# Kernel optimization log

Hardware: AMD Instinct MI355X
Metric: run time of the kernel (lower is better)

The kernel has to match this reference:

```python
import jax, jax.numpy as jnp
import numpy as np

N_KNOTS = 10
NEXPERTS = 1
NC = 8
STEP = 1.0 / (N_KNOTS - 1.0)
BN_EPS = 1e-5


def _spline_matrix(n, step):
    # natural cubic spline second-derivative solve matrix (precalc in torch code)
    mat = 4.0 * np.eye(n - 2)
    np.fill_diagonal(mat[1:, :-1], 1.0)
    np.fill_diagonal(mat[:-1, 1:], 1.0)
    A = 6.0 * np.linalg.inv(mat) / step ** 2
    z = np.zeros((1, n - 2))
    A = np.vstack([z, A, z])                      # [n, n-2]
    B = np.zeros((n - 2, n))
    np.fill_diagonal(B, 1.0)
    np.fill_diagonal(B[:, 1:], -2.0)
    np.fill_diagonal(B[:, 2:], 1.0)
    return jnp.asarray(A @ B, dtype=jnp.float32)  # [n, n]


def _conv(x, w, b, stride=2):
    y = jax.lax.conv_general_dilated(x, w, (stride, stride), 'VALID',
                                     dimension_numbers=('NCHW', 'OIHW', 'NCHW'))
    return y + b[None, :, None, None]


def _bn(x, g, be):
    # training-mode batchnorm (module default)
    m = x.mean(axis=(0, 2, 3), keepdims=True)
    v = x.var(axis=(0, 2, 3), keepdims=True)
    return g[None, :, None, None] * (x - m) * jax.lax.rsqrt(v + BN_EPS) + be[None, :, None, None]


def _interpolate(ys, mat):
    # ys: [..., n] -> cubic coeffs a,b,c,d each [..., n-1]
    h = STEP
    M = jnp.einsum('ij,...j->...i', mat, ys)
    a = (M[..., 1:] - M[..., :-1]) / (6.0 * h)
    b = M[..., :-1] / 2.0
    c = (ys[..., 1:] - ys[..., :-1]) / h - (M[..., 1:] + 2.0 * M[..., :-1]) * (h / 6.0)
    d = ys[..., :-1]
    return a, b, c, d


def _apply(coeffs, x):
    # coeffs: 4-tuple each [..., n-1]; x: [..., P] with matching leading dims
    a, b, c, d = coeffs
    xi = jnp.clip(jnp.floor(x / STEP), 0.0, N_KNOTS - 2.0)
    xf = x - xi * STEP
    idx = xi.astype(jnp.int32)
    ag = jnp.take_along_axis(a, idx, axis=-1)
    bg = jnp.take_along_axis(b, idx, axis=-1)
    cg = jnp.take_along_axis(c, idx, axis=-1)
    dg = jnp.take_along_axis(d, idx, axis=-1)
    return ((ag * xf + bg) * xf + cg) * xf + dg


def forward(x, w1, b1, w2, b2, g2, be2, w3, b3, g3, be3, w4, b4, g4, be4,
            w5, b5, g5, be5, fc1_w, fc1_b, fc2_w, fc2_b):
    B, C, H, W = x.shape
    small = x if (H, W) == (256, 256) else jax.image.resize(x, (B, C, 256, 256), 'bilinear')
    h = jax.nn.relu(_conv(small, w1, b1))
    h = _bn(jax.nn.relu(_conv(h, w2, b2)), g2, be2)
    h = _bn(jax.nn.relu(_conv(h, w3, b3)), g3, be3)
    h = _bn(jax.nn.relu(_conv(h, w4, b4)), g4, be4)
    h = _bn(jax.nn.relu(_conv(h, w5, b5)), g5, be5)   # [B, 16nc, 7, 7]
    h = h.mean(axis=(2, 3))                            # avgpool 7 -> [B, 16nc]
    h = jax.nn.relu(h @ fc1_w.T + fc1_b)
    ys = (h @ fc2_w.T + fc2_b).reshape(B, NEXPERTS, 3, N_KNOTS)
    identity = jnp.arange(N_KNOTS, dtype=jnp.float32) / (N_KNOTS - 1.0)
    ysn = ys + identity                                # residual spline
    mat = _spline_matrix(N_KNOTS, STEP)
    coeffs = _interpolate(ysn, mat)                    # each [B,E,3,n-1]
    # per-pixel spline eval at original resolution
    px = jnp.broadcast_to(x.reshape(B, 1, 3, H * W), (B, NEXPERTS, 3, H * W))
    out = _apply(coeffs, px).reshape(B, NEXPERTS, 3, H, W)
    out = jnp.transpose(out, (1, 0, 2, 3, 4))          # [E,B,3,H,W]
    # spline curves sampled at xs = arange(0,1,1/255) (255 points; detached in torch)
    xs = jnp.arange(0.0, 1.0, 1.0 / 255.0, dtype=jnp.float32)
    xs_b = jnp.broadcast_to(xs, (B, NEXPERTS, 3, xs.shape[0]))
    splines = jnp.transpose(_apply(coeffs, xs_b), (1, 0, 2, 3))  # [E,B,3,255]
    return out, splines


def setup_inputs() -> dict:
    key = jax.random.key(0)
    ks = jax.random.split(key, 16)
    n, nc, E = N_KNOTS, NC, NEXPERTS
    d = {}
    d['x'] = jax.random.uniform(ks[0], (8, 3, 1024, 1024), dtype=jnp.float32)
    d['w1'] = jax.random.normal(ks[1], (nc, 3, 3, 3), jnp.float32) * 0.1
    d['b1'] = jnp.zeros((nc,), jnp.float32)
    chans = [nc, 2 * nc, 4 * nc, 8 * nc, 16 * nc]
    for i, (ci, co) in enumerate(zip(chans[:-1], chans[1:]), start=2):
        d[f'w{i}'] = jax.random.normal(ks[i], (co, ci, 3, 3), jnp.float32) * 0.1
        d[f'b{i}'] = jnp.zeros((co,), jnp.float32)
        d[f'g{i}'] = jnp.ones((co,), jnp.float32)
        d[f'be{i}'] = jnp.zeros((co,), jnp.float32)
    d['fc1_w'] = jax.random.normal(ks[10], (16 * nc, 16 * nc), jnp.float32) * 0.05
    d['fc1_b'] = jnp.zeros((16 * nc,), jnp.float32)
    d['fc2_w'] = jax.random.normal(ks[11], (3 * n * E, 16 * nc), jnp.float32) * 0.05
    d['fc2_b'] = jnp.zeros((3 * n * E,), jnp.float32)
    return d


def reference(x, w1, b1, w2, b2, g2, be2, w3, b3, g3, be3, w4, b4, g4, be4,
              w5, b5, g5, be5, fc1_w, fc1_b, fc2_w, fc2_b):
    return forward(x, w1, b1, w2, b2, g2, be2, w3, b3, g3, be3, w4, b4, g4, be4,
                   w5, b5, g5, be5, fc1_w, fc1_b, fc2_w, fc2_b)
```

## Files before the change

### kernel.cpp

```cpp
#include <hip/hip_runtime.h>

#define SPLINE_OFF 25165824
#define STEP_F (1.0f/9.0f)

typedef float f32x4 __attribute__((ext_vector_type(4)));

__global__ __launch_bounds__(256) void resize_k(const float* __restrict__ x,
                                                float* __restrict__ sm) {
    __shared__ float vsum[1024];
    const int blk = blockIdx.x;
    const int plane = blk >> 8;
    const int orow = blk & 255;
    const int t = threadIdx.x;

    const float W[8] = {0.125f,0.375f,0.625f,0.875f,0.875f,0.625f,0.375f,0.125f};
    const float* p = x + (size_t)plane * 1048576 + t * 4;
    const int r0 = 4 * orow - 2;
    float ax = 0.f, ay = 0.f, az = 0.f, aw = 0.f;
    if (r0 >= 0 && r0 + 7 <= 1023) {
        #pragma unroll
        for (int k = 0; k < 8; k++) {
            const float4 v = *(const float4*)(p + (r0 + k) * 1024);
            const float w = W[k] * 0.25f;
            ax = fmaf(v.x, w, ax); ay = fmaf(v.y, w, ay);
            az = fmaf(v.z, w, az); aw = fmaf(v.w, w, aw);
        }
    } else {
        float wsum = 0.f;
        #pragma unroll
        for (int k = 0; k < 8; k++) {
            const int r = r0 + k;
            if (r >= 0 && r < 1024) {
                const float4 v = *(const float4*)(p + r * 1024);
                ax = fmaf(v.x, W[k], ax); ay = fmaf(v.y, W[k], ay);
                az = fmaf(v.z, W[k], az); aw = fmaf(v.w, W[k], aw);
                wsum += W[k];
            }
        }
        const float inv = 1.f / wsum;
        ax *= inv; ay *= inv; az *= inv; aw *= inv;
    }
    vsum[4 * t + 0] = ax; vsum[4 * t + 1] = ay;
    vsum[4 * t + 2] = az; vsum[4 * t + 3] = aw;
    __syncthreads();

    const int c0 = 4 * t - 2;
    float acc = 0.f;
    if (c0 >= 0 && c0 + 7 <= 1023) {
        #pragma unroll
        for (int k = 0; k < 8; k++)
            acc = fmaf(vsum[c0 + k], W[k] * 0.25f, acc);
    } else {
        float wsum = 0.f;
        #pragma unroll
        for (int k = 0; k < 8; k++) {
            const int c = c0 + k;
            if (c >= 0 && c < 1024) { acc = fmaf(vsum[c], W[k], acc); wsum += W[k]; }
        }
        acc /= wsum;
    }
    sm[(size_t)blk * 256 + t] = acc;
}

template<int CIN, int COUT, int INW, int OUTW, int NCO, int CISPLIT, int PIX,
         int NTPREV, int NTOUT, bool INBN, bool STATS, bool WRITE>
__global__ __launch_bounds__(PIX * CISPLIT) void conv_k(
    const float* __restrict__ in, const float* __restrict__ w,
    const float* __restrict__ bias,
    const float* __restrict__ gam, const float* __restrict__ be,
    const float* __restrict__ pS, const float* __restrict__ pQ, float invN,
    float* __restrict__ out,
    float* __restrict__ pSo, float* __restrict__ pQo)
{
    constexpr int BLOCK = PIX * CISPLIT;
    constexpr int CPS = CIN / CISPLIT;
    constexpr int COG = COUT / NCO;

    __shared__ float wsm[NCO][CIN * 9];
    __shared__ float scs[CIN], shs[CIN];
    __shared__ float wrow[NCO][CIN];
    __shared__ float cadd[NCO];
    __shared__ float part[CISPLIT][PIX][NCO];
    __shared__ float red[NCO][2][PIX / 64];
    __shared__ float sredS[BLOCK], sredQ[BLOCK];

    const int tid = threadIdx.x;
    const int p   = tid & (PIX - 1);
    const int cs  = tid / PIX;
    const int bc  = blockIdx.y;
    const int b   = bc / COG;
    const int co0 = (bc % COG) * NCO;

    if constexpr (INBN) {
        constexpr int GRP = BLOCK / CIN;
        constexpr int TERMS = 8 * NTPREV;
        const int ci = tid % CIN;
        const int gi = tid / CIN;
        float s = 0.f, q = 0.f;
        for (int j = gi; j < TERMS; j += GRP) {
            const int bb = j / NTPREV, tl = j - bb * NTPREV;
            const int a = (bb * CIN + ci) * NTPREV + tl;
            s += pS[a]; q += pQ[a];
        }
        sredS[gi * CIN + ci] = s;
        sredQ[gi * CIN + ci] = q;
        __syncthreads();
        if (tid < CIN) {
            float ts = 0.f, tq = 0.f;
            #pragma unroll
            for (int g2 = 0; g2 < GRP; g2++) {
                ts += sredS[g2 * CIN + tid];
                tq += sredQ[g2 * CIN + tid];
            }
            const float m = ts * invN;
            const float v = tq * invN - m * m;
            const float sc = gam[tid] * rsqrtf(v + 1e-5f);
            scs[tid] = sc;
            shs[tid] = be[tid] - m * sc;
        }
        __syncthreads();
    }

    for (int i = tid; i < NCO * CIN * 9; i += BLOCK) {
        int n = i / (CIN * 9), r = i - n * (CIN * 9), ci = r / 9;
        float wv = w[(co0 + n) * CIN * 9 + r];
        wsm[n][r] = INBN ? wv * scs[ci] : wv;
    }
    if constexpr (INBN) {
        for (int i = tid; i < NCO * CIN; i += BLOCK) {
            int n = i / CIN, ci = i - n * CIN;
            const float* wp = w + ((co0 + n) * CIN + ci) * 9;
            float s = 0.f;
            #pragma unroll
            for (int k = 0; k < 9; k++) s += wp[k];
            wrow[n][ci] = s;
        }
    }
    __syncthreads();
    if (tid < NCO) {
        float c = bias[co0 + tid];
        if constexpr (INBN) {
            for (int ci = 0; ci < CIN; ci++) c = fmaf(wrow[tid][ci], shs[ci], c);
        }
        cadd[tid] = c;
    }
    __syncthreads();

    const int npix = OUTW * OUTW;
    const int pg = blockIdx.x * PIX + p;
    float acc[NCO];
    #pragma unroll
    for (int n = 0; n < NCO; n++) acc[n] = 0.f;

    if (pg < npix) {
        const int oh = pg / OUTW, ow = pg - oh * OUTW;
        const float* ib = in + ((size_t)(b * CIN) + cs * CPS) * INW * INW
                             + (size_t)(2 * oh) * INW + 2 * ow;
        #pragma unroll 4
        for (int ci = 0; ci < CPS; ci++) {
            const float* ip = ib + (size_t)ci * INW * INW;
            const int cw = (cs * CPS + ci) * 9;
            #pragma unroll
            for (int kh = 0; kh < 3; kh++) {
                const float* r = ip + kh * INW;
                #pragma unroll
                for (int kw = 0; kw < 3; kw++) {
                    const float xv = r[kw];
                    #pragma unroll
                    for (int n = 0; n < NCO; n++)
                        acc[n] = fmaf(xv, wsm[n][cw + kh * 3 + kw], acc[n]);
                }
            }
        }
    }

    float val[NCO];
    #pragma unroll
    for (int n = 0; n < NCO; n++) val[n] = 0.f;

    if constexpr (CISPLIT > 1) {
        #pragma unroll
        for (int n = 0; n < NCO; n++) part[cs][p][n] = acc[n];
        __syncthreads();
    }

    if (cs == 0) {
        #pragma unroll
        for (int n = 0; n < NCO; n++) {
            float s = acc[n];
            if constexpr (CISPLIT > 1) {
                #pragma unroll
                for (int q = 1; q < CISPLIT; q++) s += part[q][p][n];
            }
            if (pg < npix) {
                val[n] = fmaxf(s + cadd[n], 0.f);
                if constexpr (WRITE)
                    out[(size_t)(b * COUT + co0 + n) * npix + pg] = val[n];
            }
        }
    }

    if constexpr (STATS) {
        if (cs == 0) {
            #pragma unroll
            for (int n = 0; n < NCO; n++) {
                float s = val[n], sq = val[n] * val[n];
                #pragma unroll
                for (int off = 32; off > 0; off >>= 1) {
                    s  += __shfl_down(s, off);
                    sq += __shfl_down(sq, off);
                }
                if ((tid & 63) == 0) { red[n][0][tid >> 6] = s; red[n][1][tid >> 6] = sq; }
            }
        }
        __syncthreads();
        if (tid == 0) {
            #pragma unroll
            for (int n = 0; n < NCO; n++) {
                float ts = 0.f, tq = 0.f;
                #pragma unroll
                for (int i = 0; i < PIX / 64; i++) { ts += red[n][0][i]; tq += red[n][1][i]; }
                const int idx = (b * COUT + co0 + n) * NTOUT + blockIdx.x;
                pSo[idx] = ts;
                pQo[idx] = tq;
            }
        }
    }
}

__global__ __launch_bounds__(256) void fc_spline_k(
    const float* __restrict__ pS5, const float* __restrict__ pQ5,
    const float* __restrict__ g5, const float* __restrict__ be5,
    const float* __restrict__ fc1w, const float* __restrict__ fc1b,
    const float* __restrict__ fc2w, const float* __restrict__ fc2b,
    float* __restrict__ coeff_out, float* __restrict__ splines_out)
{
    __shared__ float sc5[128], sh5[128];
    __shared__ float h[1024];
    __shared__ float h1v[1024];
    __shared__ float ysn[240];
    __shared__ float coef[24][36];

    const int t = threadIdx.x;

    if (t < 128) {
        float s = 0.f, q = 0.f;
        #pragma unroll
        for (int b = 0; b < 8; b++) { s += pS5[b * 128 + t]; q += pQ5[b * 128 + t]; }
        float m = s * (1.f / 392.f);
        float v = q * (1.f / 392.f) - m * m;
        float sc = g5[t] * rsqrtf(v + 1e-5f);
        sc5[t] = sc;
        sh5[t] = be5[t] - m * sc;
    }
    __syncthreads();

    for (int i = t; i < 1024; i += 256) {
        int c = i & 127;
        h[i] = fmaf(sc5[c], pS5[i] * (1.f / 49.f), sh5[c]);
    }
    __syncthreads();

    for (int i = t; i < 1024; i += 256) {
        int b = i >> 7, j = i & 127;
        float acc = fc1b[j];
        for (int c = 0; c < 128; c++)
            acc = fmaf(h[(b << 7) + c], fc1w[(j << 7) + c], acc);
        h1v[i] = fmaxf(acc, 0.f);
    }
    __syncthreads();

    if (t < 240) {
        int b = t / 30, k = t % 30;
        float acc = fc2b[k];
        for (int j = 0; j < 128; j++)
            acc = fmaf(h1v[(b << 7) + j], fc2w[(k << 7) + j], acc);
        ysn[t] = acc + (float)(k % 10) * STEP_F;
    }
    __syncthreads();

    if (t < 24) {
        float y[10];
        #pragma unroll
        for (int i = 0; i < 10; i++) y[i] = ysn[t * 10 + i];
        float rhs[9], cp[9], dp[9];
        #pragma unroll
        for (int i = 1; i <= 8; i++)
            rhs[i] = 486.f * (y[i - 1] - 2.f * y[i] + y[i + 1]);
        cp[1] = 0.25f; dp[1] = rhs[1] * 0.25f;
        #pragma unroll
        for (int i = 2; i <= 8; i++) {
            float m = 1.f / (4.f - cp[i - 1]);
            cp[i] = m;
            dp[i] = (rhs[i] - dp[i - 1]) * m;
        }
        float M[10];
        M[0] = 0.f; M[9] = 0.f;
        M[8] = dp[8];
        #pragma unroll
        for (int i = 7; i >= 1; i--) M[i] = dp[i] - cp[i] * M[i + 1];
        #pragma unroll
        for (int i = 0; i < 9; i++) {
            float a = (M[i + 1] - M[i]) * 1.5f;
            float bb = M[i] * 0.5f;
            float cc = (y[i + 1] - y[i]) * 9.f - (M[i + 1] + 2.f * M[i]) * (STEP_F / 6.f);
            float dd = y[i];
            coef[t][i] = a; coef[t][9 + i] = bb; coef[t][18 + i] = cc; coef[t][27 + i] = dd;
            coeff_out[t * 36 + i] = a;
            coeff_out[t * 36 + 9 + i] = bb;
            coeff_out[t * 36 + 18 + i] = cc;
            coeff_out[t * 36 + 27 + i] = dd;
        }
    }
    __syncthreads();

    for (int i = t; i < 24 * 255; i += 256) {
        int bc = i / 255, k = i - bc * 255;
        float xv = (float)k * (1.0f / 255.0f);
        float xi = floorf(xv * 9.0f);
        xi = fminf(fmaxf(xi, 0.f), 8.f);
        int ix = (int)xi;
        float xf = xv - xi * STEP_F;
        const float* cf = coef[bc];
        splines_out[i] = fmaf(fmaf(fmaf(cf[ix], xf, cf[9 + ix]), xf, cf[18 + ix]), xf, cf[27 + ix]);
    }
}

__global__ __launch_bounds__(256) void apply_k(const float* __restrict__ x,
                                               const float* __restrict__ coeff,
                                               float* __restrict__ out)
{
    __shared__ float cf[36];
    const int blk = blockIdx.x;
    const int plane = blk >> 10;
    const int t = threadIdx.x;
    if (t < 36) cf[t] = coeff[plane * 36 + t];
    __syncthreads();

    size_t base = (size_t)blk * 1024 + (size_t)t * 4;
    float4 v = *(const float4*)(x + base);
    f32x4 o;
    #pragma unroll
    for (int k = 0; k < 4; k++) {
        float xv = (k == 0) ? v.x : (k == 1) ? v.y : (k == 2) ? v.z : v.w;
        float xi = floorf(xv * 9.0f);
        xi = fminf(fmaxf(xi, 0.f), 8.f);
        int ix = (int)xi;
        float xf = xv - xi * STEP_F;
        o[k] = fmaf(fmaf(fmaf(cf[ix], xf, cf[9 + ix]), xf, cf[18 + ix]), xf, cf[27 + ix]);
    }
    __builtin_nontemporal_store(o, (f32x4*)(out + base));
}

extern "C" void kernel_launch(void* const* d_in, const int* in_sizes, int n_in,
                              void* d_out, int out_size, void* d_ws, size_t ws_size,
                              hipStream_t stream) {
    (void)in_sizes; (void)n_in; (void)out_size; (void)ws_size;

    const float* x    = (const float*)d_in[0];
    const float* w1   = (const float*)d_in[1];
    const float* b1   = (const float*)d_in[2];
    const float* w2   = (const float*)d_in[3];
    const float* b2   = (const float*)d_in[4];
    const float* g2   = (const float*)d_in[5];
    const float* be2  = (const float*)d_in[6];
    const float* w3   = (const float*)d_in[7];
    const float* b3   = (const float*)d_in[8];
    const float* g3   = (const float*)d_in[9];
    const float* be3  = (const float*)d_in[10];
    const float* w4   = (const float*)d_in[11];
    const float* b4   = (const float*)d_in[12];
    const float* g4   = (const float*)d_in[13];
    const float* be4  = (const float*)d_in[14];
    const float* w5   = (const float*)d_in[15];
    const float* b5   = (const float*)d_in[16];
    const float* g5   = (const float*)d_in[17];
    const float* be5  = (const float*)d_in[18];
    const float* fc1w = (const float*)d_in[19];
    const float* fc1b = (const float*)d_in[20];
    const float* fc2w = (const float*)d_in[21];
    const float* fc2b = (const float*)d_in[22];

    float* out = (float*)d_out;
    float* wsf = (float*)d_ws;

    float* pS2 = wsf + 0;
    float* pQ2 = wsf + 2048;
    float* pS3 = wsf + 4096;
    float* pQ3 = wsf + 5120;
    float* pS4 = wsf + 6144;
    float* pQ4 = wsf + 6656;
    float* pS5 = wsf + 7168;
    float* pQ5 = wsf + 8192;
    float* coeff = wsf + 9216;

    float* sm  = out;
    float* h1  = out + 1572864;
    float* h2  = out + 2605120;
    float* h3  = out + 3113152;
    float* h4  = out + 3359168;

    resize_k<<<6144, 256, 0, stream>>>(x, sm);

    conv_k<3, 8, 256, 127, 2, 1, 256, 1, 1, false, false, true>
        <<<dim3(64, 32), 256, 0, stream>>>(sm, w1, b1, nullptr, nullptr,
                                           nullptr, nullptr, 0.f,
                                           h1, nullptr, nullptr);
    conv_k<8, 16, 127, 63, 2, 1, 256, 1, 16, false, true, true>
        <<<dim3(16, 64), 256, 0, stream>>>(h1, w2, b2, nullptr, nullptr,
                                           nullptr, nullptr, 0.f,
                                           h2, pS2, pQ2);
    conv_k<16, 32, 63, 31, 2, 1, 256, 16, 4, true, true, true>
        <<<dim3(4, 128), 256, 0, stream>>>(h2, w3, b3, g2, be2,
                                           pS2, pQ2, 1.0f / 31752.0f,
                                           h3, pS3, pQ3);
    conv_k<32, 64, 31, 15, 2, 2, 256, 4, 1, true, true, true>
        <<<dim3(1, 256), 512, 0, stream>>>(h3, w4, b4, g3, be3,
                                           pS3, pQ3, 1.0f / 7688.0f,
                                           h4, pS4, pQ4);
    conv_k<64, 128, 15, 7, 2, 4, 64, 1, 1, true, true, false>
        <<<dim3(1, 512), 256, 0, stream>>>(h4, w5, b5, g4, be4,
                                           pS4, pQ4, 1.0f / 1800.0f,
                                           nullptr, pS5, pQ5);

    fc_spline_k<<<1, 256, 0, stream>>>(pS5, pQ5, g5, be5,
                                       fc1w, fc1b, fc2w, fc2b,
                                       coeff, out + SPLINE_OFF);

    apply_k<<<24576, 256, 0, stream>>>(x, coeff, out);
}
```

Measured before the change: 132.1 us.

## Fuse conv1 and conv2 into tiled kernel, batch resize rows, raise CI split

A new tiled kernel fuses conv1 and conv2. It stages the resized input tile and the conv1 output in shared memory, so the h1 intermediate never goes to global memory, and it emits per-tile BN statistics. The resize kernel now computes two output rows per block and shares the overlapping input rows, which cuts redundant global loads. The later convs use larger input-channel splits and therefore bigger blocks, trading more shared-memory reduction for more parallelism per block.

```diff
diff --git a/kernel.cpp b/kernel.cpp
--- a/kernel.cpp
+++ b/kernel.cpp
@@ -7,62 +7,174 @@
 
 __global__ __launch_bounds__(256) void resize_k(const float* __restrict__ x,
                                                 float* __restrict__ sm) {
-    __shared__ float vsum[1024];
+    __shared__ float vs[2][1024];
     const int blk = blockIdx.x;
-    const int plane = blk >> 8;
-    const int orow = blk & 255;
+    const int plane = blk >> 7;
+    const int orA = (blk & 127) * 2;
     const int t = threadIdx.x;
 
     const float W[8] = {0.125f,0.375f,0.625f,0.875f,0.875f,0.625f,0.375f,0.125f};
     const float* p = x + (size_t)plane * 1048576 + t * 4;
-    const int r0 = 4 * orow - 2;
-    float ax = 0.f, ay = 0.f, az = 0.f, aw = 0.f;
-    if (r0 >= 0 && r0 + 7 <= 1023) {
-        #pragma unroll
-        for (int k = 0; k < 8; k++) {
-            const float4 v = *(const float4*)(p + (r0 + k) * 1024);
-            const float w = W[k] * 0.25f;
-            ax = fmaf(v.x, w, ax); ay = fmaf(v.y, w, ay);
-            az = fmaf(v.z, w, az); aw = fmaf(v.w, w, aw);
+    const int rA = 4 * orA - 2;
+
+    float a0x=0.f,a0y=0.f,a0z=0.f,a0w=0.f;
+    float a1x=0.f,a1y=0.f,a1z=0.f,a1w=0.f;
+
+    if (rA >= 0 && rA + 11 <= 1023) {
+        #pragma unroll
+        for (int k = 0; k < 12; k++) {
+            const float4 v = *(const float4*)(p + (size_t)(rA + k) * 1024);
+            if (k < 8) {
+                const float w = W[k] * 0.25f;
+                a0x = fmaf(v.x, w, a0x); a0y = fmaf(v.y, w, a0y);
+                a0z = fmaf(v.z, w, a0z); a0w = fmaf(v.w, w, a0w);
+            }
+            if (k >= 4) {
+                const float w = W[k - 4] * 0.25f;
+                a1x = fmaf(v.x, w, a1x); a1y = fmaf(v.y, w, a1y);
+                a1z = fmaf(v.z, w, a1z); a1w = fmaf(v.w, w, a1w);
+            }
         }
     } else {
-        float wsum = 0.f;
-        #pragma unroll
-        for (int k = 0; k < 8; k++) {
-            const int r = r0 + k;
-            if (r >= 0 && r < 1024) {
-                const float4 v = *(const float4*)(p + r * 1024);
-                ax = fmaf(v.x, W[k], ax); ay = fmaf(v.y, W[k], ay);
-                az = fmaf(v.z, W[k], az); aw = fmaf(v.w, W[k], aw);
-                wsum += W[k];
-            }
-        }
-        const float inv = 1.f / wsum;
-        ax *= inv; ay *= inv; az *= inv; aw *= inv;
-    }
-    vsum[4 * t + 0] = ax; vsum[4 * t + 1] = ay;
-    vsum[4 * t + 2] = az; vsum[4 * t + 3] = aw;
+        #pragma unroll
+        for (int o = 0; o < 2; o++) {
+            const int r0 = 4 * (orA + o) - 2;
+            float bx=0.f,by=0.f,bz=0.f,bw=0.f,wsum=0.f;
+            #pragma unroll
+            for (int k = 0; k < 8; k++) {
+                const int r = r0 + k;
+                if (r >= 0 && r < 1024) {
+                    const float4 v = *(const float4*)(p + (size_t)r * 1024);
+                    bx = fmaf(v.x, W[k], bx); by = fmaf(v.y, W[k], by);
+                    bz = fmaf(v.z, W[k], bz); bw = fmaf(v.w, W[k], bw);
+                    wsum += W[k];
+                }
+            }
+            const float inv = 1.f / wsum;
+            if (o == 0) { a0x=bx*inv; a0y=by*inv; a0z=bz*inv; a0w=bw*inv; }
+            else        { a1x=bx*inv; a1y=by*inv; a1z=bz*inv; a1w=bw*inv; }
+        }
+    }
+    vs[0][4*t+0]=a0x; vs[0][4*t+1]=a0y; vs[0][4*t+2]=a0z; vs[0][4*t+3]=a0w;
+    vs[1][4*t+0]=a1x; vs[1][4*t+1]=a1y; vs[1][4*t+2]=a1z; vs[1][4*t+3]=a1w;
     __syncthreads();
 
     const int c0 = 4 * t - 2;
-    float acc = 0.f;
-    if (c0 >= 0 && c0 + 7 <= 1023) {
-        #pragma unroll
-        for (int k = 0; k < 8; k++)
-            acc = fmaf(vsum[c0 + k], W[k] * 0.25f, acc);
-    } else {
-        float wsum = 0.f;
-        #pragma unroll
-        for (int k = 0; k < 8; k++) {
-            const int c = c0 + k;
-            if (c >= 0 && c < 1024) { acc = fmaf(vsum[c], W[k], acc); wsum += W[k]; }
-        }
-        acc /= wsum;
-    }
-    sm[(size_t)blk * 256 + t] = acc;
+    #pragma unroll
+    for (int o = 0; o < 2; o++) {
+        float acc = 0.f;
+        if (c0 >= 0 && c0 + 7 <= 1023) {
+            #pragma unroll
+            for (int k = 0; k < 8; k++)
+                acc = fmaf(vs[o][c0 + k], W[k] * 0.25f, acc);
+        } else {
+            float wsum = 0.f;
+            #pragma unroll
+            for (int k = 0; k < 8; k++) {
+                const int c = c0 + k;
+                if (c >= 0 && c < 1024) { acc = fmaf(vs[o][c], W[k], acc); wsum += W[k]; }
+            }
+            acc /= wsum;
+        }
+        sm[((size_t)plane * 256 + orA + o) * 256 + t] = acc;
+    }
 }
 
-template<int CIN, int COUT, int INW, int OUTW, int NCO, int CISPLIT, int PIX,
+__global__ __launch_bounds__(256) void c1c2_k(
+    const float* __restrict__ sm,
+    const float* __restrict__ w1, const float* __restrict__ b1,
+    const float* __restrict__ w2, const float* __restrict__ b2,
+    float* __restrict__ h2, float* __restrict__ pS2, float* __restrict__ pQ2)
+{
+    __shared__ float smT[3 * 1225];
+    __shared__ float c1T[8 * 289];
+    __shared__ float w1s[216];
+    __shared__ float w2s[1152];
+    __shared__ float bs[24];
+
+    const int tile = blockIdx.x;
+    const int b    = blockIdx.y;
+    const int tx = tile & 7, ty = tile >> 3;
+    const int R0 = ty * 8, C0 = tx * 8;
+    const int t = threadIdx.x;
+
+    if (t < 216) w1s[t] = w1[t];
+    for (int i = t; i < 1152; i += 256) w2s[i] = w2[i];
+    if (t < 8) bs[t] = b1[t];
+    else if (t < 24) bs[t] = b2[t - 8];
+
+    const int r0 = 4 * R0, c0 = 4 * C0;
+    for (int i = t; i < 3675; i += 256) {
+        const int ch = i / 1225, rem = i - ch * 1225;
+        const int r = rem / 35, c = rem - r * 35;
+        const int gr = r0 + r, gc = c0 + c;
+        float v = 0.f;
+        if (gr < 256 && gc < 256)
+            v = sm[((size_t)(b * 3 + ch) << 16) + (gr << 8) + gc];
+        smT[i] = v;
+    }
+    __syncthreads();
+
+    for (int i = t; i < 2312; i += 256) {
+        const int co = i / 289, pp = i - co * 289;
+        const int r = pp / 17, c = pp - r * 17;
+        float acc = bs[co];
+        #pragma unroll
+        for (int ch = 0; ch < 3; ch++) {
+            const float* sp = &smT[ch * 1225 + (2 * r) * 35 + 2 * c];
+            const float* wp = &w1s[co * 27 + ch * 9];
+            #pragma unroll
+            for (int kh = 0; kh < 3; kh++) {
+                acc = fmaf(sp[kh * 35 + 0], wp[kh * 3 + 0], acc);
+                acc = fmaf(sp[kh * 35 + 1], wp[kh * 3 + 1], acc);
+                acc = fmaf(sp[kh * 35 + 2], wp[kh * 3 + 2], acc);
+            }
+        }
+        c1T[i] = fmaxf(acc, 0.f);
+    }
+    __syncthreads();
+
+    const int px = t & 63, cog = t >> 6;
+    const int pr = px >> 3, pc = px & 7;
+    const bool valid = (R0 + pr < 63) && (C0 + pc < 63);
+    float vals[4];
+    #pragma unroll
+    for (int k = 0; k < 4; k++) {
+        const int co = cog * 4 + k;
+        float acc = bs[8 + co];
+        #pragma unroll
+        for (int ci = 0; ci < 8; ci++) {
+            const float* cp = &c1T[ci * 289 + (2 * pr) * 17 + 2 * pc];
+            const float* wp = &w2s[co * 72 + ci * 9];
+            #pragma unroll
+            for (int kh = 0; kh < 3; kh++) {
+                acc = fmaf(cp[kh * 17 + 0], wp[kh * 3 + 0], acc);
+                acc = fmaf(cp[kh * 17 + 1], wp[kh * 3 + 1], acc);
+                acc = fmaf(cp[kh * 17 + 2], wp[kh * 3 + 2], acc);
+            }
+        }
+        const float v = valid ? fmaxf(acc, 0.f) : 0.f;
+        vals[k] = v;
+        if (valid)
+            h2[(size_t)(b * 16 + co) * 3969 + (R0 + pr) * 63 + (C0 + pc)] = v;
+    }
+    #pragma unroll
+    for (int k = 0; k < 4; k++) {
+        float s = vals[k], q = vals[k] * vals[k];
+        #pragma unroll
+        for (int off = 32; off > 0; off >>= 1) {
+            s += __shfl_down(s, off);
+            q += __shfl_down(q, off);
+        }
+        if (px == 0) {
+            const int co = cog * 4 + k;
+            pS2[(b * 16 + co) * 64 + tile] = s;
+            pQ2[(b * 16 + co) * 64 + tile] = q;
+        }
+    }
+}
+
+template<int CIN, int COUT, int INW, int OUTW, int CISPLIT, int PIX,
          int NTPREV, int NTOUT, bool INBN, bool STATS, bool WRITE>
 __global__ __launch_bounds__(PIX * CISPLIT) void conv_k(
     const float* __restrict__ in, const float* __restrict__ w,
@@ -74,14 +186,14 @@
 {
     constexpr int BLOCK = PIX * CISPLIT;
     constexpr int CPS = CIN / CISPLIT;
-    constexpr int COG = COUT / NCO;
-
-    __shared__ float wsm[NCO][CIN * 9];
+    constexpr int COG = COUT / 2;
+
+    __shared__ float wsm[2][CIN * 9];
     __shared__ float scs[CIN], shs[CIN];
-    __shared__ float wrow[NCO][CIN];
-    __shared__ float cadd[NCO];
-    __shared__ float part[CISPLIT][PIX][NCO];
-    __shared__ float red[NCO][2][PIX / 64];
+    __shared__ float wrow[2][CIN];
+    __shared__ float cadd[2];
+    __shared__ float part[CISPLIT][PIX][2];
+    __shared__ float red[2][2][PIX / 64];
     __shared__ float sredS[BLOCK], sredQ[BLOCK];
 
     const int tid = threadIdx.x;
@@ -89,7 +201,7 @@
     const int cs  = tid / PIX;
     const int bc  = blockIdx.y;
     const int b   = bc / COG;
-    const int co0 = (bc % COG) * NCO;
+    const int co0 = (bc % COG) * 2;
 
     if constexpr (INBN) {
         constexpr int GRP = BLOCK / CIN;
@@ -121,14 +233,14 @@
         __syncthreads();
     }
 
-    for (int i = tid; i < NCO * CIN * 9; i += BLOCK) {
-        int n = i / (CIN * 9), r = i - n * (CIN * 9), ci = r / 9;
-        float wv = w[(co0 + n) * CIN * 9 + r];
+    for (int i = tid; i < 2 * CIN * 9; i += BLOCK) {
+        const int n = i / (CIN * 9), r = i - n * (CIN * 9), ci = r / 9;
+        const float wv = w[(co0 + n) * CIN * 9 + r];
         wsm[n][r] = INBN ? wv * scs[ci] : wv;
     }
     if constexpr (INBN) {
-        for (int i = tid; i < NCO * CIN; i += BLOCK) {
-            int n = i / CIN, ci = i - n * CIN;
+        for (int i = tid; i < 2 * CIN; i += BLOCK) {
+            const int n = i / CIN, ci = i - n * CIN;
             const float* wp = w + ((co0 + n) * CIN + ci) * 9;
             float s = 0.f;
             #pragma unroll
@@ -137,7 +249,7 @@
         }
     }
     __syncthreads();
-    if (tid < NCO) {
+    if (tid < 2) {
         float c = bias[co0 + tid];
         if constexpr (INBN) {
             for (int ci = 0; ci < CIN; ci++) c = fmaf(wrow[tid][ci], shs[ci], c);
@@ -148,17 +260,14 @@
 
     const int npix = OUTW * OUTW;
     const int pg = blockIdx.x * PIX + p;
-    float acc[NCO];
-    #pragma unroll
-    for (int n = 0; n < NCO; n++) acc[n] = 0.f;
-
+    float a0 = 0.f, a1 = 0.f;
     if (pg < npix) {
         const int oh = pg / OUTW, ow = pg - oh * OUTW;
-        const float* ib = in + ((size_t)(b * CIN) + cs * CPS) * INW * INW
+        const float* ib = in + ((size_t)(b * CIN) + cs * CPS) * (INW * INW)
                              + (size_t)(2 * oh) * INW + 2 * ow;
         #pragma unroll 4
         for (int ci = 0; ci < CPS; ci++) {
-            const float* ip = ib + (size_t)ci * INW * INW;
+            const float* ip = ib + (size_t)ci * (INW * INW);
             const int cw = (cs * CPS + ci) * 9;
             #pragma unroll
             for (int kh = 0; kh < 3; kh++) {
@@ -166,64 +275,59 @@
                 #pragma unroll
                 for (int kw = 0; kw < 3; kw++) {
                     const float xv = r[kw];
-                    #pragma unroll
-                    for (int n = 0; n < NCO; n++)
-                        acc[n] = fmaf(xv, wsm[n][cw + kh * 3 + kw], acc[n]);
+                    a0 = fmaf(xv, wsm[0][cw + kh * 3 + kw], a0);
+                    a1 = fmaf(xv, wsm[1][cw + kh * 3 + kw], a1);
                 }
             }
         }
     }
 
-    float val[NCO];
-    #pragma unroll
-    for (int n = 0; n < NCO; n++) val[n] = 0.f;
-
+    float v0 = 0.f, v1 = 0.f;
     if constexpr (CISPLIT > 1) {
-        #pragma unroll
-        for (int n = 0; n < NCO; n++) part[cs][p][n] = acc[n];
+        part[cs][p][0] = a0; part[cs][p][1] = a1;
         __syncthreads();
     }
-
     if (cs == 0) {
-        #pragma unroll
-        for (int n = 0; n < NCO; n++) {
-            float s = acc[n];
-            if constexpr (CISPLIT > 1) {
-                #pragma unroll
-                for (int q = 1; q < CISPLIT; q++) s += part[q][p][n];
-            }
-            if (pg < npix) {
-                val[n] = fmaxf(s + cadd[n], 0.f);
-                if constexpr (WRITE)
-                    out[(size_t)(b * COUT + co0 + n) * npix + pg] = val[n];
+        float s0 = a0, s1 = a1;
+        if constexpr (CISPLIT > 1) {
+            #pragma unroll
+            for (int q = 1; q < CISPLIT; q++) { s0 += part[q][p][0]; s1 += part[q][p][1]; }
+        }
+        if (pg < npix) {
+            v0 = fmaxf(s0 + cadd[0], 0.f);
+            v1 = fmaxf(s1 + cadd[1], 0.f);
+            if constexpr (WRITE) {
+                out[(size_t)(b * COUT + co0) * npix + pg] = v0;
+                out[(size_t)(b * COUT + co0 + 1) * npix + pg] = v1;
             }
         }
     }
 
     if constexpr (STATS) {
         if (cs == 0) {
-            #pragma unroll
-            for (int n = 0; n < NCO; n++) {
-                float s = val[n], sq = val[n] * val[n];
-                #pragma unroll
-                for (int off = 32; off > 0; off >>= 1) {
-                    s  += __shfl_down(s, off);
-                    sq += __shfl_down(sq, off);
-                }
-                if ((tid & 63) == 0) { red[n][0][tid >> 6] = s; red[n][1][tid >> 6] = sq; }
+            float sA = v0, qA = v0 * v0, sB = v1, qB = v1 * v1;
+            #pragma unroll
+            for (int off = 32; off > 0; off >>= 1) {
+                sA += __shfl_down(sA, off); qA += __shfl_down(qA, off);
+                sB += __shfl_down(sB, off); qB += __shfl_down(qB, off);
+            }
+            if ((tid & 63) == 0) {
+                red[0][0][tid >> 6] = sA; red[0][1][tid >> 6] = qA;
+                red[1][0][tid >> 6] = sB; red[1][1][tid >> 6] = qB;
             }
         }
         __syncthreads();
         if (tid == 0) {
-            #pragma unroll
-            for (int n = 0; n < NCO; n++) {
-                float ts = 0.f, tq = 0.f;
-                #pragma unroll
-                for (int i = 0; i < PIX / 64; i++) { ts += red[n][0][i]; tq += red[n][1][i]; }
-                const int idx = (b * COUT + co0 + n) * NTOUT + blockIdx.x;
-                pSo[idx] = ts;
-                pQo[idx] = tq;
-            }
+            float tsA = 0.f, tqA = 0.f, tsB = 0.f, tqB = 0.f;
+            #pragma unroll
+            for (int i = 0; i < PIX / 64; i++) {
+                tsA += red[0][0][i]; tqA += red[0][1][i];
+                tsB += red[1][0][i]; tqB += red[1][1][i];
+            }
+            pSo[(b * COUT + co0) * NTOUT + blockIdx.x] = tsA;
+            pQo[(b * COUT + co0) * NTOUT + blockIdx.x] = tqA;
+            pSo[(b * COUT + co0 + 1) * NTOUT + blockIdx.x] = tsB;
+            pQo[(b * COUT + co0 + 1) * NTOUT + blockIdx.x] = tqB;
         }
     }
 }
@@ -385,41 +489,34 @@
     float* wsf = (float*)d_ws;
 
     float* pS2 = wsf + 0;
-    float* pQ2 = wsf + 2048;
-    float* pS3 = wsf + 4096;
-    float* pQ3 = wsf + 5120;
-    float* pS4 = wsf + 6144;
-    float* pQ4 = wsf + 6656;
-    float* pS5 = wsf + 7168;
-    float* pQ5 = wsf + 8192;
-    float* coeff = wsf + 9216;
+    float* pQ2 = wsf + 8192;
+    float* pS3 = wsf + 16384;
+    float* pQ3 = wsf + 17408;
+    float* pS4 = wsf + 18432;
+    float* pQ4 = wsf + 18944;
+    float* pS5 = wsf + 19456;
+    float* pQ5 = wsf + 20480;
+    float* coeff = wsf + 21504;
 
     float* sm  = out;
-    float* h1  = out + 1572864;
-    float* h2  = out + 2605120;
-    float* h3  = out + 3113152;
-    float* h4  = out + 3359168;
-
-    resize_k<<<6144, 256, 0, stream>>>(x, sm);
-
-    conv_k<3, 8, 256, 127, 2, 1, 256, 1, 1, false, false, true>
-        <<<dim3(64, 32), 256, 0, stream>>>(sm, w1, b1, nullptr, nullptr,
-                                           nullptr, nullptr, 0.f,
-                                           h1, nullptr, nullptr);
-    conv_k<8, 16, 127, 63, 2, 1, 256, 1, 16, false, true, true>
-        <<<dim3(16, 64), 256, 0, stream>>>(h1, w2, b2, nullptr, nullptr,
-                                           nullptr, nullptr, 0.f,
-                                           h2, pS2, pQ2);
-    conv_k<16, 32, 63, 31, 2, 1, 256, 16, 4, true, true, true>
-        <<<dim3(4, 128), 256, 0, stream>>>(h2, w3, b3, g2, be2,
+    float* h2  = out + 1572864;
+    float* h3  = out + 2080896;
+    float* h4  = out + 2326912;
+
+    resize_k<<<3072, 256, 0, stream>>>(x, sm);
+
+    c1c2_k<<<dim3(64, 8), 256, 0, stream>>>(sm, w1, b1, w2, b2, h2, pS2, pQ2);
+
+    conv_k<16, 32, 63, 31, 2, 256, 64, 4, true, true, true>
+        <<<dim3(4, 128), 512, 0, stream>>>(h2, w3, b3, g2, be2,
                                            pS2, pQ2, 1.0f / 31752.0f,
                                            h3, pS3, pQ3);
-    conv_k<32, 64, 31, 15, 2, 2, 256, 4, 1, true, true, true>
-        <<<dim3(1, 256), 512, 0, stream>>>(h3, w4, b4, g3, be3,
-                                           pS3, pQ3, 1.0f / 7688.0f,
-                                           h4, pS4, pQ4);
-    conv_k<64, 128, 15, 7, 2, 4, 64, 1, 1, true, true, false>
-        <<<dim3(1, 512), 256, 0, stream>>>(h4, w5, b5, g4, be4,
+    conv_k<32, 64, 31, 15, 4, 256, 4, 1, true, true, true>
+        <<<dim3(1, 256), 1024, 0, stream>>>(h3, w4, b4, g3, be3,
+                                            pS3, pQ3, 1.0f / 7688.0f,
+                                            h4, pS4, pQ4);
+    conv_k<64, 128, 15, 7, 8, 64, 1, 1, true, true, false>
+        <<<dim3(1, 512), 512, 0, stream>>>(h4, w5, b5, g4, be4,
                                            pS4, pQ4, 1.0f / 1800.0f,
                                            nullptr, pS5, pQ5);
 
```

New measurement: 145.1 us. 1.1x slower.
